# Kernel tuning notes

Measured on AMD Instinct MI355X. Metric: run time of the kernel, lower is better.

The kernel has to match this reference:

```python
import jax, jax.numpy as jnp
import numpy as np

B = 1024      # batch
G = 2000      # num_genes
S = 32        # uniform per-gene feature width (geneid_num[i] == 32 for all i)
M1, M2, M3 = 4096, 2048, 1024  # mul_len1/2/3
H = 64        # hidden width of all small MLPs


def setup_inputs() -> dict:
    key = jax.random.key(0)
    ks = jax.random.split(key, 24)
    n = lambda k, shape, s=0.02: jax.random.normal(k, shape, dtype=jnp.float32) * s
    return {
        # activations
        "x":  jax.random.normal(ks[0], (B, G * S), dtype=jnp.float32),
        "z1": jax.random.normal(ks[1], (B, M1), dtype=jnp.float32),
        "z2": jax.random.normal(ks[2], (B, M2), dtype=jnp.float32),
        "z3": jax.random.normal(ks[3], (B, M3), dtype=jnp.float32),
        # per-gene Linear(S,1) weights, stacked: block-diagonal gene stage
        "Wg": n(ks[4], (G, S)), "bg": n(ks[5], (G,)),
        # fc0: Linear(G, 64); fc1/2/3: Linear(Mi, 64). Layout (in, out).
        "W0": n(ks[6], (G, H)),  "b0": n(ks[7], (H,)),
        "W1": n(ks[8], (M1, H)), "b1": n(ks[9], (H,)),
        "W2": n(ks[10], (M2, H)), "b2": n(ks[11], (H,)),
        "W3": n(ks[12], (M3, H)), "b3": n(ks[13], (H,)),
        # learned fusion weights (init 0.5 in torch)
        "w1": jnp.full((H,), 0.5, jnp.float32),
        "w2": jnp.full((H,), 0.5, jnp.float32),
        "w3": jnp.full((H,), 0.5, jnp.float32),
        # final fc: 64->64->64->1
        "fW1": n(ks[14], (H, H)), "fb1": n(ks[15], (H,)),
        "fW2": n(ks[16], (H, H)), "fb2": n(ks[17], (H,)),
        "fW3": n(ks[18], (H, 1)), "fb3": n(ks[19], (1,)),
    }


def reference(x, z1, z2, z3, Wg, bg, W0, b0, W1, b1, W2, b2, W3, b3,
              w1, w2, w3, fW1, fb1, fW2, fb2, fW3, fb3):
    g, s = Wg.shape
    b = x.shape[0]
    # ragged per-gene Linear(numi,1)+ReLU loop == block-diagonal contraction
    # x: [B, G*S] -> [B, G, S]; gene_outputs: [B, G]
    gene = jax.nn.relu(jnp.einsum('bgs,gs->bg', x.reshape(b, g, s), Wg) + bg)
    h0 = jax.nn.relu(gene @ W0 + b0)                 # fc0(gene_outputs)  [B, 64]
    d1 = jax.nn.relu(z1 @ W1 + b1) * w1 + h0         # fc1(z1)*weights_1 + fc0
    d2 = jax.nn.relu(z2 @ W2 + b2) * w2 + d1         # fc2(z2)*weights_2 + d1
    d3 = jax.nn.relu(z3 @ W3 + b3) * w3 + d2         # fc3(z3)*weights_3 + d2
    h = jax.nn.relu(d3 @ fW1 + fb1)
    h = jax.nn.relu(h @ fW2 + fb2)
    return h @ fW3 + fb3                             # [B, 1]
```

## Files before the change

kernel.cpp:

```cpp
#include <hip/hip_runtime.h>

constexpr int BB = 1024;
constexpr int GG = 2000;
constexpr int SS = 32;
constexpr int K1 = 4096, K2 = 2048, K3 = 1024;
constexpr int HH = 64;

constexpr int BH      = BB * HH;
constexpr int GENE_SZ = BB * GG;
constexpr int Y1P_OFF = GENE_SZ;
constexpr int Y2P_OFF = Y1P_OFF + 4 * BH;
constexpr int Y3P_OFF = Y2P_OFF + 2 * BH;

constexpr int NGENE_CHUNKS = 63;
constexpr int NB_GRP       = 16;
constexpr int NGENE_BLK    = NGENE_CHUNKS * NB_GRP;
constexpr int NGEMM_BLK    = 448;
constexpr int KCH          = 1024;

__global__ __launch_bounds__(256, 4) void k1_gene_and_zgemm(
    const float* __restrict__ x,  const float* __restrict__ z1,
    const float* __restrict__ z2, const float* __restrict__ z3,
    const float* __restrict__ Wg, const float* __restrict__ bg,
    const float* __restrict__ W1, const float* __restrict__ W2,
    const float* __restrict__ W3, float* __restrict__ ws)
{
    __shared__ float zt[16 * 64];
    const int bid = blockIdx.x;
    const int t   = threadIdx.x;

    const int per = bid / 13;
    const int off = bid % 13;

    if (off >= 4) {
        const int gid   = per * 9 + (off - 4);
        const int chunk = gid % NGENE_CHUNKS;
        const int bgrp  = gid / NGENE_CHUNKS;
        const int g0    = chunk * 32;
        const int b0    = bgrp * 64;
        const int g     = g0 + (t >> 3);
        const bool gv   = (g < GG);

        float4 wg4 = make_float4(0.f, 0.f, 0.f, 0.f);
        if (gv) wg4 = ((const float4*)Wg)[g0 * 8 + t];
        float bias = 0.f;
        if (gv && (t & 7) == 0) bias = bg[g];

        const float* xp = gv ? (x + (size_t)b0 * (GG * SS) + g0 * SS + t * 4)
                             : x;
        float* gene = ws;

        #pragma unroll 4
        for (int i = 0; i < 64; ++i) {
            float4 x4 = *(const float4*)(xp + (size_t)i * (GG * SS));
            float p = x4.x * wg4.x + x4.y * wg4.y + x4.z * wg4.z + x4.w * wg4.w;
            p += __shfl_xor(p, 1);
            p += __shfl_xor(p, 2);
            p += __shfl_xor(p, 4);
            if (gv && (t & 7) == 0)
                gene[(size_t)(b0 + i) * GG + g] = fmaxf(p + bias, 0.f);
        }
    } else {
        const int id = per * 4 + off;
        const float* z; const float* W; int K; int mt; float* ys; int kbase;
        if (id < 256)      { z = z1; W = W1; K = K1; mt = id >> 2; kbase = (id & 3) * KCH;
                             ys = ws + Y1P_OFF + (size_t)(id & 3) * BH; }
        else if (id < 384) { int l = id - 256; z = z2; W = W2; K = K2; mt = l >> 1; kbase = (l & 1) * KCH;
                             ys = ws + Y2P_OFF + (size_t)(l & 1) * BH; }
        else               { int l = id - 384; z = z3; W = W3; K = K3; mt = l; kbase = 0;
                             ys = ws + Y3P_OFF; }

        const int m0 = mt * 16;
        const int n  = t & 63;
        const int w  = t >> 6;
        const int srow = t >> 4;
        const int scol = (t & 15) * 4;

        float a0 = 0.f, a1 = 0.f, a2 = 0.f, a3 = 0.f;

        for (int kc = 0; kc < KCH / 64; ++kc) {
            const int k0 = kbase + kc * 64;
            *(float4*)&zt[srow * 64 + scol] =
                *(const float4*)&z[(size_t)(m0 + srow) * K + k0 + scol];
            __syncthreads();
            #pragma unroll
            for (int kk = 0; kk < 64; kk += 4) {
                const float* Wp = W + (size_t)(k0 + kk) * 64 + n;
                const float wa = Wp[0], wb = Wp[64], wc = Wp[128], wd = Wp[192];
                const float4 za = *(const float4*)&zt[(w * 4 + 0) * 64 + kk];
                const float4 zb = *(const float4*)&zt[(w * 4 + 1) * 64 + kk];
                const float4 zc = *(const float4*)&zt[(w * 4 + 2) * 64 + kk];
                const float4 zd = *(const float4*)&zt[(w * 4 + 3) * 64 + kk];
                a0 = fmaf(za.w, wd, fmaf(za.z, wc, fmaf(za.y, wb, fmaf(za.x, wa, a0))));
                a1 = fmaf(zb.w, wd, fmaf(zb.z, wc, fmaf(zb.y, wb, fmaf(zb.x, wa, a1))));
                a2 = fmaf(zc.w, wd, fmaf(zc.z, wc, fmaf(zc.y, wb, fmaf(zc.x, wa, a2))));
                a3 = fmaf(zd.w, wd, fmaf(zd.z, wc, fmaf(zd.y, wb, fmaf(zd.x, wa, a3))));
            }
            __syncthreads();
        }
        ys[(size_t)(m0 + w * 4 + 0) * 64 + n] = a0;
        ys[(size_t)(m0 + w * 4 + 1) * 64 + n] = a1;
        ys[(size_t)(m0 + w * 4 + 2) * 64 + n] = a2;
        ys[(size_t)(m0 + w * 4 + 3) * 64 + n] = a3;
    }
}

__global__ __launch_bounds__(256, 4) void k2_fc0_combine_mlp(
    const float* __restrict__ ws,
    const float* __restrict__ W0,  const float* __restrict__ b0v,
    const float* __restrict__ b1v, const float* __restrict__ b2v,
    const float* __restrict__ b3v,
    const float* __restrict__ w1v, const float* __restrict__ w2v,
    const float* __restrict__ w3v,
    const float* __restrict__ fW1, const float* __restrict__ fb1,
    const float* __restrict__ fW2, const float* __restrict__ fb2,
    const float* __restrict__ fW3, const float* __restrict__ fb3,
    float* __restrict__ out)
{
    const float* gene = ws;
    const float* Y1p  = ws + Y1P_OFF;
    const float* Y2p  = ws + Y2P_OFF;
    const float* Y3p  = ws + Y3P_OFF;

    const int t   = threadIdx.x;
    const int n   = t & 63;
    const int w   = t >> 6;
    const int row = blockIdx.x * 4 + w;

    float acc = 0.f;
    const float* gp = gene + (size_t)row * GG;
    #pragma unroll 4
    for (int k = 0; k < GG; k += 4) {
        const float4 g4 = *(const float4*)(gp + k);
        const float* Wp = W0 + (size_t)k * 64 + n;
        acc = fmaf(g4.w, Wp[192], fmaf(g4.z, Wp[128],
              fmaf(g4.y, Wp[64],  fmaf(g4.x, Wp[0], acc))));
    }
    const float h0 = fmaxf(acc + b0v[n], 0.f);

    const int rn = row * 64 + n;
    const float y1 = Y1p[rn] + Y1p[BH + rn] + Y1p[2 * BH + rn] + Y1p[3 * BH + rn];
    float d = fmaf(fmaxf(y1 + b1v[n], 0.f), w1v[n], h0);
    const float y2 = Y2p[rn] + Y2p[BH + rn];
    d = fmaf(fmaxf(y2 + b2v[n], 0.f), w2v[n], d);
    const float y3 = Y3p[rn];
    d = fmaf(fmaxf(y3 + b3v[n], 0.f), w3v[n], d);

    __shared__ float sd[4][64];
    __shared__ float sh[4][64];
    sd[w][n] = d;
    __syncthreads();
    float a1 = fb1[n];
    #pragma unroll 8
    for (int j = 0; j < 64; ++j) a1 = fmaf(sd[w][j], fW1[j * 64 + n], a1);
    a1 = fmaxf(a1, 0.f);
    sh[w][n] = a1;
    __syncthreads();
    float a2 = fb2[n];
    #pragma unroll 8
    for (int j = 0; j < 64; ++j) a2 = fmaf(sh[w][j], fW2[j * 64 + n], a2);
    a2 = fmaxf(a2, 0.f);

    float v = a2 * fW3[n];
    #pragma unroll
    for (int o = 32; o > 0; o >>= 1) v += __shfl_xor(v, o);
    if (n == 0) out[row] = v + fb3[0];
}

extern "C" void kernel_launch(void* const* d_in, const int* in_sizes, int n_in,
                              void* d_out, int out_size, void* d_ws, size_t ws_size,
                              hipStream_t stream)
{
    const float* x   = (const float*)d_in[0];
    const float* z1  = (const float*)d_in[1];
    const float* z2  = (const float*)d_in[2];
    const float* z3  = (const float*)d_in[3];
    const float* Wg  = (const float*)d_in[4];
    const float* bg  = (const float*)d_in[5];
    const float* W0  = (const float*)d_in[6];
    const float* b0v = (const float*)d_in[7];
    const float* W1  = (const float*)d_in[8];
    const float* b1v = (const float*)d_in[9];
    const float* W2  = (const float*)d_in[10];
    const float* b2v = (const float*)d_in[11];
    const float* W3  = (const float*)d_in[12];
    const float* b3v = (const float*)d_in[13];
    const float* w1v = (const float*)d_in[14];
    const float* w2v = (const float*)d_in[15];
    const float* w3v = (const float*)d_in[16];
    const float* fW1 = (const float*)d_in[17];
    const float* fb1 = (const float*)d_in[18];
    const float* fW2 = (const float*)d_in[19];
    const float* fb2 = (const float*)d_in[20];
    const float* fW3 = (const float*)d_in[21];
    const float* fb3 = (const float*)d_in[22];

    float* ws  = (float*)d_ws;
    float* out = (float*)d_out;

    k1_gene_and_zgemm<<<dim3(NGENE_BLK + NGEMM_BLK), dim3(256), 0, stream>>>(
        x, z1, z2, z3, Wg, bg, W1, W2, W3, ws);

    k2_fc0_combine_mlp<<<dim3(BB / 4), dim3(256), 0, stream>>>(
        ws, W0, b0v, b1v, b2v, b3v, w1v, w2v, w3v,
        fW1, fb1, fW2, fb2, fW3, fb3, out);
}
```

Before: 504.8 us.

## Fuse fc0 partial GEMM into gene blocks and retile z-GEMMs to 32 rows

Each gene block now keeps its 64x32 gene tile in LDS and immediately multiplies it by the matching 32 rows of W0. It writes a per-chunk partial of h0, so the [B,G] gene matrix never goes to global memory. The second kernel only sums 63 partials instead of running a 2000-long dot per row. The z-GEMM blocks are retiled to 32 rows with 2 outputs per thread, halving block count and W reloads. The cost is extra workspace traffic for 63 partial buffers (63*BH floats) and more registers for the W0 slice.

```diff
diff --git a/kernel.cpp b/kernel.cpp
--- a/kernel.cpp
+++ b/kernel.cpp
@@ -4,38 +4,37 @@
 constexpr int GG = 2000;
 constexpr int SS = 32;
 constexpr int K1 = 4096, K2 = 2048, K3 = 1024;
-constexpr int HH = 64;
-
-constexpr int BH      = BB * HH;
-constexpr int GENE_SZ = BB * GG;
-constexpr int Y1P_OFF = GENE_SZ;
-constexpr int Y2P_OFF = Y1P_OFF + 4 * BH;
-constexpr int Y3P_OFF = Y2P_OFF + 2 * BH;
-
-constexpr int NGENE_CHUNKS = 63;
-constexpr int NB_GRP       = 16;
-constexpr int NGENE_BLK    = NGENE_CHUNKS * NB_GRP;
-constexpr int NGEMM_BLK    = 448;
-constexpr int KCH          = 1024;
-
-__global__ __launch_bounds__(256, 4) void k1_gene_and_zgemm(
+
+constexpr int BH = BB * 64;
+
+constexpr int Y1P_OFF = 0;
+constexpr int Y2P_OFF = 4 * BH;
+constexpr int Y3P_OFF = 6 * BH;
+constexpr int HP_OFF  = 7 * BH;
+
+constexpr int NCH       = 63;
+constexpr int NGENE_BLK = NCH * 16;
+constexpr int NGEMM_BLK = 224;
+constexpr int KCH       = 1024;
+
+__global__ __launch_bounds__(256, 4) void k1_gene_fc0_zgemm(
     const float* __restrict__ x,  const float* __restrict__ z1,
     const float* __restrict__ z2, const float* __restrict__ z3,
     const float* __restrict__ Wg, const float* __restrict__ bg,
+    const float* __restrict__ W0,
     const float* __restrict__ W1, const float* __restrict__ W2,
     const float* __restrict__ W3, float* __restrict__ ws)
 {
-    __shared__ float zt[16 * 64];
+    __shared__ float lds[64 * 32];
     const int bid = blockIdx.x;
     const int t   = threadIdx.x;
-
-    const int per = bid / 13;
-    const int off = bid % 13;
-
-    if (off >= 4) {
-        const int gid   = per * 9 + (off - 4);
-        const int chunk = gid % NGENE_CHUNKS;
-        const int bgrp  = gid / NGENE_CHUNKS;
+    const int per = bid / 11;
+    const int off = bid % 11;
+
+    if (off >= 2) {
+        const int gid   = per * 9 + (off - 2);
+        const int chunk = gid % NCH;
+        const int bgrp  = gid / NCH;
         const int g0    = chunk * 32;
         const int b0    = bgrp * 64;
         const int g     = g0 + (t >> 3);
@@ -43,12 +42,11 @@
 
         float4 wg4 = make_float4(0.f, 0.f, 0.f, 0.f);
         if (gv) wg4 = ((const float4*)Wg)[g0 * 8 + t];
-        float bias = 0.f;
-        if (gv && (t & 7) == 0) bias = bg[g];
+        const float bias = (gv && (t & 7) == 0) ? bg[g] : 0.f;
 
         const float* xp = gv ? (x + (size_t)b0 * (GG * SS) + g0 * SS + t * 4)
                              : x;
-        float* gene = ws;
+        float* gS = lds;
 
         #pragma unroll 4
         for (int i = 0; i < 64; ++i) {
@@ -57,57 +55,88 @@
             p += __shfl_xor(p, 1);
             p += __shfl_xor(p, 2);
             p += __shfl_xor(p, 4);
-            if (gv && (t & 7) == 0)
-                gene[(size_t)(b0 + i) * GG + g] = fmaxf(p + bias, 0.f);
+            if ((t & 7) == 0)
+                gS[i * 32 + (t >> 3)] = gv ? fmaxf(p + bias, 0.f) : 0.f;
+        }
+
+        const int n = t & 63;
+        const int w = t >> 6;
+        float w0r[32];
+        #pragma unroll
+        for (int j = 0; j < 32; ++j) {
+            int gj = g0 + j; if (gj >= GG) gj = GG - 1;
+            w0r[j] = W0[(size_t)gj * 64 + n];
+        }
+        __syncthreads();
+
+        float* hp = ws + HP_OFF + (size_t)chunk * BH + (size_t)b0 * 64;
+        #pragma unroll 4
+        for (int mi = 0; mi < 16; ++mi) {
+            const int m = w * 16 + mi;
+            float acc = 0.f;
+            #pragma unroll
+            for (int jj = 0; jj < 8; ++jj) {
+                const float4 g4 = *(const float4*)&gS[m * 32 + jj * 4];
+                acc = fmaf(g4.w, w0r[jj * 4 + 3], fmaf(g4.z, w0r[jj * 4 + 2],
+                      fmaf(g4.y, w0r[jj * 4 + 1], fmaf(g4.x, w0r[jj * 4 + 0], acc))));
+            }
+            hp[(size_t)m * 64 + n] = acc;
         }
     } else {
-        const int id = per * 4 + off;
-        const float* z; const float* W; int K; int mt; float* ys; int kbase;
-        if (id < 256)      { z = z1; W = W1; K = K1; mt = id >> 2; kbase = (id & 3) * KCH;
-                             ys = ws + Y1P_OFF + (size_t)(id & 3) * BH; }
-        else if (id < 384) { int l = id - 256; z = z2; W = W2; K = K2; mt = l >> 1; kbase = (l & 1) * KCH;
-                             ys = ws + Y2P_OFF + (size_t)(l & 1) * BH; }
-        else               { int l = id - 384; z = z3; W = W3; K = K3; mt = l; kbase = 0;
+        const int id = per * 2 + off;
+        const float* z; const float* W; int K; int mt; int kslab; float* ys;
+        if (id < 128)      { z = z1; W = W1; K = K1; mt = id >> 2; kslab = id & 3;
+                             ys = ws + Y1P_OFF + (size_t)kslab * BH; }
+        else if (id < 192) { int l = id - 128; z = z2; W = W2; K = K2; mt = l >> 1; kslab = l & 1;
+                             ys = ws + Y2P_OFF + (size_t)kslab * BH; }
+        else               { int l = id - 192; z = z3; W = W3; K = K3; mt = l; kslab = 0;
                              ys = ws + Y3P_OFF; }
 
-        const int m0 = mt * 16;
-        const int n  = t & 63;
-        const int w  = t >> 6;
-        const int srow = t >> 4;
-        const int scol = (t & 15) * 4;
-
-        float a0 = 0.f, a1 = 0.f, a2 = 0.f, a3 = 0.f;
+        const int m0    = mt * 32;
+        const int kbase = kslab * KCH;
+        const int n2    = t & 31;
+        const int mq    = t >> 5;
+        float* zt = lds;
+
+        float2 acc[4];
+        #pragma unroll
+        for (int j = 0; j < 4; ++j) acc[j] = make_float2(0.f, 0.f);
 
         for (int kc = 0; kc < KCH / 64; ++kc) {
             const int k0 = kbase + kc * 64;
-            *(float4*)&zt[srow * 64 + scol] =
-                *(const float4*)&z[(size_t)(m0 + srow) * K + k0 + scol];
+            {
+                const int i0 = t, i1 = t + 256;
+                ((float4*)zt)[i0] = *(const float4*)&z[(size_t)(m0 + (i0 >> 4)) * K + k0 + (i0 & 15) * 4];
+                ((float4*)zt)[i1] = *(const float4*)&z[(size_t)(m0 + (i1 >> 4)) * K + k0 + (i1 & 15) * 4];
+            }
             __syncthreads();
             #pragma unroll
             for (int kk = 0; kk < 64; kk += 4) {
-                const float* Wp = W + (size_t)(k0 + kk) * 64 + n;
-                const float wa = Wp[0], wb = Wp[64], wc = Wp[128], wd = Wp[192];
-                const float4 za = *(const float4*)&zt[(w * 4 + 0) * 64 + kk];
-                const float4 zb = *(const float4*)&zt[(w * 4 + 1) * 64 + kk];
-                const float4 zc = *(const float4*)&zt[(w * 4 + 2) * 64 + kk];
-                const float4 zd = *(const float4*)&zt[(w * 4 + 3) * 64 + kk];
-                a0 = fmaf(za.w, wd, fmaf(za.z, wc, fmaf(za.y, wb, fmaf(za.x, wa, a0))));
-                a1 = fmaf(zb.w, wd, fmaf(zb.z, wc, fmaf(zb.y, wb, fmaf(zb.x, wa, a1))));
-                a2 = fmaf(zc.w, wd, fmaf(zc.z, wc, fmaf(zc.y, wb, fmaf(zc.x, wa, a2))));
-                a3 = fmaf(zd.w, wd, fmaf(zd.z, wc, fmaf(zd.y, wb, fmaf(zd.x, wa, a3))));
+                const float* Wp = &W[(size_t)(k0 + kk) * 64 + n2 * 2];
+                const float2 wv0 = *(const float2*)(Wp);
+                const float2 wv1 = *(const float2*)(Wp + 64);
+                const float2 wv2 = *(const float2*)(Wp + 128);
+                const float2 wv3 = *(const float2*)(Wp + 192);
+                #pragma unroll
+                for (int j = 0; j < 4; ++j) {
+                    const float4 zj = *(const float4*)&zt[(mq * 4 + j) * 64 + kk];
+                    acc[j].x = fmaf(zj.x, wv0.x, acc[j].x); acc[j].y = fmaf(zj.x, wv0.y, acc[j].y);
+                    acc[j].x = fmaf(zj.y, wv1.x, acc[j].x); acc[j].y = fmaf(zj.y, wv1.y, acc[j].y);
+                    acc[j].x = fmaf(zj.z, wv2.x, acc[j].x); acc[j].y = fmaf(zj.z, wv2.y, acc[j].y);
+                    acc[j].x = fmaf(zj.w, wv3.x, acc[j].x); acc[j].y = fmaf(zj.w, wv3.y, acc[j].y);
+                }
             }
             __syncthreads();
         }
-        ys[(size_t)(m0 + w * 4 + 0) * 64 + n] = a0;
-        ys[(size_t)(m0 + w * 4 + 1) * 64 + n] = a1;
-        ys[(size_t)(m0 + w * 4 + 2) * 64 + n] = a2;
-        ys[(size_t)(m0 + w * 4 + 3) * 64 + n] = a3;
+        #pragma unroll
+        for (int j = 0; j < 4; ++j)
+            *(float2*)&ys[(size_t)(m0 + mq * 4 + j) * 64 + n2 * 2] = acc[j];
     }
 }
 
-__global__ __launch_bounds__(256, 4) void k2_fc0_combine_mlp(
+__global__ __launch_bounds__(256, 4) void k2_combine_mlp(
     const float* __restrict__ ws,
-    const float* __restrict__ W0,  const float* __restrict__ b0v,
+    const float* __restrict__ b0v,
     const float* __restrict__ b1v, const float* __restrict__ b2v,
     const float* __restrict__ b3v,
     const float* __restrict__ w1v, const float* __restrict__ w2v,
@@ -117,28 +146,22 @@
     const float* __restrict__ fW3, const float* __restrict__ fb3,
     float* __restrict__ out)
 {
-    const float* gene = ws;
-    const float* Y1p  = ws + Y1P_OFF;
-    const float* Y2p  = ws + Y2P_OFF;
-    const float* Y3p  = ws + Y3P_OFF;
+    const float* Y1p = ws + Y1P_OFF;
+    const float* Y2p = ws + Y2P_OFF;
+    const float* Y3p = ws + Y3P_OFF;
 
     const int t   = threadIdx.x;
     const int n   = t & 63;
     const int w   = t >> 6;
     const int row = blockIdx.x * 4 + w;
-
-    float acc = 0.f;
-    const float* gp = gene + (size_t)row * GG;
-    #pragma unroll 4
-    for (int k = 0; k < GG; k += 4) {
-        const float4 g4 = *(const float4*)(gp + k);
-        const float* Wp = W0 + (size_t)k * 64 + n;
-        acc = fmaf(g4.w, Wp[192], fmaf(g4.z, Wp[128],
-              fmaf(g4.y, Wp[64],  fmaf(g4.x, Wp[0], acc))));
-    }
-    const float h0 = fmaxf(acc + b0v[n], 0.f);
-
-    const int rn = row * 64 + n;
+    const int rn  = row * 64 + n;
+
+    float h = 0.f;
+    const float* hp = ws + HP_OFF + rn;
+    #pragma unroll 9
+    for (int c = 0; c < NCH; ++c) h += hp[(size_t)c * BH];
+    const float h0 = fmaxf(h + b0v[n], 0.f);
+
     const float y1 = Y1p[rn] + Y1p[BH + rn] + Y1p[2 * BH + rn] + Y1p[3 * BH + rn];
     float d = fmaf(fmaxf(y1 + b1v[n], 0.f), w1v[n], h0);
     const float y2 = Y2p[rn] + Y2p[BH + rn];
@@ -198,10 +221,10 @@
     float* ws  = (float*)d_ws;
     float* out = (float*)d_out;
 
-    k1_gene_and_zgemm<<<dim3(NGENE_BLK + NGEMM_BLK), dim3(256), 0, stream>>>(
-        x, z1, z2, z3, Wg, bg, W1, W2, W3, ws);
-
-    k2_fc0_combine_mlp<<<dim3(BB / 4), dim3(256), 0, stream>>>(
-        ws, W0, b0v, b1v, b2v, b3v, w1v, w2v, w3v,
+    k1_gene_fc0_zgemm<<<dim3(NGENE_BLK + NGEMM_BLK), dim3(256), 0, stream>>>(
+        x, z1, z2, z3, Wg, bg, W0, W1, W2, W3, ws);
+
+    k2_combine_mlp<<<dim3(BB / 4), dim3(256), 0, stream>>>(
+        ws, b0v, b1v, b2v, b3v, w1v, w2v, w3v,
         fW1, fb1, fW2, fb2, fW3, fb3, out);
 }
```

New measurement: 488.0 us. -3.3%, faster.
